# Kernel tuning notes

Measured on AMD Instinct MI355X. Metric: run time of the kernel, lower is better.

Reference implementation:

```python
import jax, jax.numpy as jnp
import numpy as np

N = 100000
E_RAND = 800000
IN_D, HID_D, OUT_D = 128, 64, 64
PROP_STEP = 8
ATTN_AFT = PROP_STEP // 2  # attention applied after this many prop steps
LAM = 1.0
ALP = 1.0 / (LAM + 1.0)    # alp=0 in init -> DGL auto-sets 1/(lam+1)
TAU = 0.2
P_RHO = 1.0
T_UP = -1.0                # T<=0 -> no upper threshold


def setup_inputs() -> dict:
    key = jax.random.key(0)
    k1, k2, k3, k4, k5 = jax.random.split(key, 5)
    loops = jnp.arange(N)
    src = jnp.concatenate([jax.random.randint(k1, (E_RAND,), 0, N), loops]).astype(jnp.int32)
    dst = jnp.concatenate([jax.random.randint(k2, (E_RAND,), 0, N), loops]).astype(jnp.int32)
    feat = jax.random.normal(k3, (N, IN_D), jnp.float32)
    # xavier_normal init, zero bias (as in MLP.reset_params)
    W_bef = jax.random.normal(k4, (IN_D, HID_D), jnp.float32) * np.float32(np.sqrt(2.0 / (IN_D + HID_D)))
    b_bef = jnp.zeros((HID_D,), jnp.float32)
    W_aft = jax.random.normal(k5, (HID_D, OUT_D), jnp.float32) * np.float32(np.sqrt(2.0 / (HID_D + OUT_D)))
    b_aft = jnp.zeros((OUT_D,), jnp.float32)
    return {"feat": feat, "W_bef": W_bef, "b_bef": b_bef, "W_aft": W_aft, "b_aft": b_aft, "src": src, "dst": dst}


def _ax(src, dst, w, X):
    # Y = A X with per-edge weights: scatter-add of w_e * X[src_e] into dst_e
    return jax.ops.segment_sum(X[src] * w[:, None], dst, num_segments=N)


def _attention(src, dst, Y):
    hs, hd = Y[src], Y[dst]  # [E, d]
    w = jnp.sum(hs * hs, -1) + jnp.sum(hd * hd, -1) - 2.0 * jnp.sum(hs * hd, -1)  # ||h_u - h_v||^2
    w = jax.nn.relu(w) + 1e-7
    w = jnp.power(w, 1.0 - 0.5 * P_RHO)
    w = jnp.maximum(w, TAU)  # lower threshold tau (in-place clamp in torch)
    if T_UP > 0:
        w = jnp.where(w > T_UP, jnp.inf, w)
    w = 1.0 / w + 1e-9
    deg = jax.ops.segment_sum(w, dst, num_segments=N)  # copy_e -> sum per dst node
    return w, deg


def _prop(src, dst, w, deg, Y, X):
    dt = LAM * deg + (1.0 - LAM)
    nrm = jnp.power(dt, -0.5)[:, None]
    py = nrm * _ax(src, dst, w, nrm * Y)
    return (1.0 - ALP) * Y + ALP * LAM * py + ALP * (X / dt[:, None])


def reference(feat, W_bef, b_bef, W_aft, b_aft, src, dst):
    X = feat @ W_bef + b_bef  # mlp_bef: single Linear(input_d, hidden_d)
    w = jnp.ones(src.shape[0], feat.dtype)  # initial edge weights = 1
    deg = jax.ops.segment_sum(w, dst, num_segments=N)  # in-degrees
    Y = X
    for k in range(PROP_STEP):
        Y = _prop(src, dst, w, deg, Y, X)
        if k == ATTN_AFT - 1:
            w, deg = _attention(src, dst, Y)
    # mlp_aft: init_activate=True (relu; norm='none', dropout=0) then Linear(hidden_d, output_d)
    return jax.nn.relu(Y) @ W_aft + b_aft
```

## Files before the change

kernel.cpp:

```cpp
#include <hip/hip_runtime.h>
#include <math.h>

#define IN_D 128
#define HID 64

typedef unsigned short ushort_t;
typedef unsigned int uint_t;

static __device__ __forceinline__ ushort_t f2bf(float f) {
    uint_t x = __float_as_uint(f);
    uint_t r = x + 0x7fffu + ((x >> 16) & 1u);
    return (ushort_t)(r >> 16);
}
static __device__ __forceinline__ float bf2f(ushort_t u) {
    return __uint_as_float(((uint_t)u) << 16);
}


__global__ void zero1_kernel(int* a, int n) {
    int i = blockIdx.x * blockDim.x + threadIdx.x;
    if (i < n) a[i] = 0;
}

__global__ void hist_kernel(const int* __restrict__ dst, int E, int* __restrict__ cnt) {
    int e = blockIdx.x * blockDim.x + threadIdx.x;
    if (e < E) atomicAdd(&cnt[dst[e]], 1);
}

__global__ void scan1_kernel(int* __restrict__ cnt, int N,
                             int* __restrict__ row_ptr, int* __restrict__ blocksum,
                             float* __restrict__ nrm, float* __restrict__ invdt) {
    __shared__ int sm[1024];
    int i = blockIdx.x * 1024 + threadIdx.x;
    int v = (i < N) ? cnt[i] : 0;
    if (i < N) {
        cnt[i] = 0;
        float d = (float)v;
        nrm[i] = 1.0f / sqrtf(d);
        invdt[i] = 1.0f / d;
    }
    sm[threadIdx.x] = v;
    __syncthreads();
    for (int off = 1; off < 1024; off <<= 1) {
        int t = (threadIdx.x >= off) ? sm[threadIdx.x - off] : 0;
        __syncthreads();
        sm[threadIdx.x] += t;
        __syncthreads();
    }
    if (i < N) row_ptr[i + 1] = sm[threadIdx.x];
    if (threadIdx.x == 1023) blocksum[blockIdx.x] = sm[1023];
}

__global__ void scan2_kernel(int* __restrict__ blocksum, int nb) {
    __shared__ int sm[1024];
    int v = (threadIdx.x < nb) ? blocksum[threadIdx.x] : 0;
    sm[threadIdx.x] = v;
    __syncthreads();
    for (int off = 1; off < 1024; off <<= 1) {
        int t = (threadIdx.x >= off) ? sm[threadIdx.x - off] : 0;
        __syncthreads();
        sm[threadIdx.x] += t;
        __syncthreads();
    }
    if (threadIdx.x < nb) blocksum[threadIdx.x] = sm[threadIdx.x] - v;
}

__global__ void scan3_kernel(int* __restrict__ row_ptr, int N, const int* __restrict__ blocksum) {
    int i = blockIdx.x * 1024 + threadIdx.x;
    if (i < N) row_ptr[i + 1] += blocksum[blockIdx.x];
    if (i == 0) row_ptr[0] = 0;
}

__global__ void scatter_kernel(const int* __restrict__ src, const int* __restrict__ dst, int E,
                               const int* __restrict__ row_ptr, int* __restrict__ cursor,
                               const float* __restrict__ nrm,
                               int* __restrict__ src_perm, int* __restrict__ dst_perm,
                               float* __restrict__ coef) {
    int e = blockIdx.x * blockDim.x + threadIdx.x;
    if (e < E) {
        int d = dst[e];
        int s = src[e];
        int pos = row_ptr[d] + atomicAdd(&cursor[d], 1);
        src_perm[pos] = s;
        dst_perm[pos] = d;
        coef[pos] = nrm[s];
    }
}

__global__ void coef_kernel(const int* __restrict__ src_perm, const float* __restrict__ w_perm,
                            const float* __restrict__ nrm, int E, float* __restrict__ coef) {
    int e = blockIdx.x * blockDim.x + threadIdx.x;
    if (e < E) coef[e] = w_perm[e] * nrm[src_perm[e]];
}


__global__ __launch_bounds__(256) void prop_kernel(
    const float* __restrict__ Yin, const ushort_t* __restrict__ Ybf,
    const float* __restrict__ X,
    const int* __restrict__ row_ptr, const int* __restrict__ src_perm,
    const float* __restrict__ coef, const float* __restrict__ nrm,
    const float* __restrict__ invdt, int N,
    float* __restrict__ Yout, ushort_t* __restrict__ Yout_bf) {
    int wave = __builtin_amdgcn_readfirstlane((blockIdx.x * blockDim.x + threadIdx.x) >> 6);
    int lane = threadIdx.x & 63;
    if (wave >= N) return;
    int r0 = row_ptr[wave], r1 = row_ptr[wave + 1];
    float acc = 0.0f;
    int j = r0;
    for (; j + 4 <= r1; j += 4) {
        float v[4], c[4];
        #pragma unroll
        for (int u = 0; u < 4; ++u) {
            int s = src_perm[j + u];
            c[u] = coef[j + u];
            v[u] = bf2f(Ybf[(size_t)s * HID + lane]);
        }
        #pragma unroll
        for (int u = 0; u < 4; ++u) acc = fmaf(c[u], v[u], acc);
    }
    if (j < r1) {
        float v[4], c[4];
        #pragma unroll
        for (int u = 0; u < 4; ++u) {
            int jj = j + u;
            int valid = jj < r1;
            int idx = valid ? jj : r1 - 1;
            int s = src_perm[idx];
            float cc = coef[idx];
            c[u] = valid ? cc : 0.0f;
            v[u] = bf2f(Ybf[(size_t)s * HID + lane]);
        }
        #pragma unroll
        for (int u = 0; u < 4; ++u) acc = fmaf(c[u], v[u], acc);
    }
    size_t base = (size_t)wave * HID + lane;
    float out = 0.5f * Yin[base] + (0.5f * nrm[wave]) * acc + (0.5f * invdt[wave]) * X[base];
    Yout[base] = out;
    Yout_bf[base] = f2bf(out);
}

__global__ __launch_bounds__(256) void attn_edge_kernel(
    const ushort_t* __restrict__ Ybf,
    const int* __restrict__ src_perm, const int* __restrict__ dst_perm,
    int E, float* __restrict__ w_perm) {
    int e = blockIdx.x * blockDim.x + threadIdx.x;
    if (e >= E) return;
    int s = src_perm[e], d = dst_perm[e];
    const uint4* ps = (const uint4*)(Ybf + (size_t)s * HID);
    const uint4* pd = (const uint4*)(Ybf + (size_t)d * HID);
    uint4 a[8], b[8];
    #pragma unroll
    for (int i = 0; i < 8; ++i) a[i] = ps[i];
    #pragma unroll
    for (int i = 0; i < 8; ++i) b[i] = pd[i];
    float ss = 0.0f;
    #pragma unroll
    for (int i = 0; i < 8; ++i) {
        const uint_t* ua = (const uint_t*)&a[i];
        const uint_t* ub = (const uint_t*)&b[i];
        #pragma unroll
        for (int j = 0; j < 4; ++j) {
            float slo = __uint_as_float(ua[j] << 16);
            float dlo = __uint_as_float(ub[j] << 16);
            float shi = __uint_as_float(ua[j] & 0xffff0000u);
            float dhi = __uint_as_float(ub[j] & 0xffff0000u);
            float t0 = slo - dlo;
            float t1 = shi - dhi;
            ss = fmaf(t0, t0, ss);
            ss = fmaf(t1, t1, ss);
        }
    }
    float w = fmaxf(ss, 0.0f) + 1e-7f;
    w = sqrtf(w);
    w = fmaxf(w, 0.2f);
    w = 1.0f / w + 1e-9f;
    w_perm[e] = w;
}

__global__ __launch_bounds__(256) void deg_sum_kernel(
    const float* __restrict__ w_perm, const int* __restrict__ row_ptr, int N,
    float* __restrict__ nrm, float* __restrict__ invdt) {
    int v = (blockIdx.x * blockDim.x + threadIdx.x) >> 6;
    int lane = threadIdx.x & 63;
    if (v >= N) return;
    int r0 = row_ptr[v], r1 = row_ptr[v + 1];
    float s = 0.0f;
    for (int j = r0 + lane; j < r1; j += 64) s += w_perm[j];
    #pragma unroll
    for (int o = 32; o >= 1; o >>= 1) s += __shfl_xor(s, o, 64);
    if (lane == 0) {
        nrm[v] = 1.0f / sqrtf(s);
        invdt[v] = 1.0f / s;
    }
}

__global__ __launch_bounds__(256) void gemm1_kernel(
    const float* __restrict__ feat, const float* __restrict__ W,
    const float* __restrict__ b, int N, float* __restrict__ X, ushort_t* __restrict__ Xbf) {
    __shared__ float Wl[IN_D * HID];
    __shared__ float featL[16 * IN_D];
    for (int i = threadIdx.x; i < IN_D * HID; i += 256) Wl[i] = W[i];
    int c = threadIdx.x & 63;
    int rsub = threadIdx.x >> 6;
    float bias = b[c];
    int ngroups = N / 16;
    const float4* feat4 = (const float4*)feat;
    for (int g = blockIdx.x; g < ngroups; g += gridDim.x) {
        __syncthreads();
        float4* fl4 = (float4*)featL;
        fl4[threadIdx.x]       = feat4[(size_t)g * 512 + threadIdx.x];
        fl4[threadIdx.x + 256] = feat4[(size_t)g * 512 + 256 + threadIdx.x];
        __syncthreads();
        const float4* f0 = (const float4*)&featL[(rsub) * IN_D];
        const float4* f1 = (const float4*)&featL[(rsub + 4) * IN_D];
        const float4* f2 = (const float4*)&featL[(rsub + 8) * IN_D];
        const float4* f3 = (const float4*)&featL[(rsub + 12) * IN_D];
        float acc0 = bias, acc1 = bias, acc2 = bias, acc3 = bias;
        #pragma unroll
        for (int k4 = 0; k4 < IN_D / 4; ++k4) {
            float4 a = f0[k4];
            float4 e = f1[k4];
            float4 h = f2[k4];
            float4 q = f3[k4];
            float w0 = Wl[(4 * k4 + 0) * HID + c];
            float w1 = Wl[(4 * k4 + 1) * HID + c];
            float w2 = Wl[(4 * k4 + 2) * HID + c];
            float w3 = Wl[(4 * k4 + 3) * HID + c];
            acc0 += a.x * w0 + a.y * w1 + a.z * w2 + a.w * w3;
            acc1 += e.x * w0 + e.y * w1 + e.z * w2 + e.w * w3;
            acc2 += h.x * w0 + h.y * w1 + h.z * w2 + h.w * w3;
            acc3 += q.x * w0 + q.y * w1 + q.z * w2 + q.w * w3;
        }
        size_t row = (size_t)g * 16;
        X[(row + rsub) * HID + c] = acc0;
        X[(row + rsub + 4) * HID + c] = acc1;
        X[(row + rsub + 8) * HID + c] = acc2;
        X[(row + rsub + 12) * HID + c] = acc3;
        Xbf[(row + rsub) * HID + c] = f2bf(acc0);
        Xbf[(row + rsub + 4) * HID + c] = f2bf(acc1);
        Xbf[(row + rsub + 8) * HID + c] = f2bf(acc2);
        Xbf[(row + rsub + 12) * HID + c] = f2bf(acc3);
    }
}

__global__ __launch_bounds__(256) void gemm2_kernel(
    const float* __restrict__ Y, const float* __restrict__ W,
    const float* __restrict__ b, int N, float* __restrict__ out) {
    __shared__ float Wl[HID * HID];
    __shared__ float Yl[16 * HID];
    for (int i = threadIdx.x; i < HID * HID; i += 256) Wl[i] = W[i];
    int c = threadIdx.x & 63;
    int rsub = threadIdx.x >> 6;
    float bias = b[c];
    int ngroups = N / 16;
    const float4* Y4 = (const float4*)Y;
    for (int g = blockIdx.x; g < ngroups; g += gridDim.x) {
        __syncthreads();
        {
            float4 v = Y4[(size_t)g * 256 + threadIdx.x];
            v.x = fmaxf(v.x, 0.0f); v.y = fmaxf(v.y, 0.0f);
            v.z = fmaxf(v.z, 0.0f); v.w = fmaxf(v.w, 0.0f);
            ((float4*)Yl)[threadIdx.x] = v;
        }
        __syncthreads();
        const float4* f0 = (const float4*)&Yl[(rsub) * HID];
        const float4* f1 = (const float4*)&Yl[(rsub + 4) * HID];
        const float4* f2 = (const float4*)&Yl[(rsub + 8) * HID];
        const float4* f3 = (const float4*)&Yl[(rsub + 12) * HID];
        float acc0 = bias, acc1 = bias, acc2 = bias, acc3 = bias;
        #pragma unroll
        for (int k4 = 0; k4 < HID / 4; ++k4) {
            float4 a = f0[k4];
            float4 e = f1[k4];
            float4 h = f2[k4];
            float4 q = f3[k4];
            float w0 = Wl[(4 * k4 + 0) * HID + c];
            float w1 = Wl[(4 * k4 + 1) * HID + c];
            float w2 = Wl[(4 * k4 + 2) * HID + c];
            float w3 = Wl[(4 * k4 + 3) * HID + c];
            acc0 += a.x * w0 + a.y * w1 + a.z * w2 + a.w * w3;
            acc1 += e.x * w0 + e.y * w1 + e.z * w2 + e.w * w3;
            acc2 += h.x * w0 + h.y * w1 + h.z * w2 + h.w * w3;
            acc3 += q.x * w0 + q.y * w1 + q.z * w2 + q.w * w3;
        }
        size_t row = (size_t)g * 16;
        out[(row + rsub) * HID + c] = acc0;
        out[(row + rsub + 4) * HID + c] = acc1;
        out[(row + rsub + 8) * HID + c] = acc2;
        out[(row + rsub + 12) * HID + c] = acc3;
    }
}


extern "C" void kernel_launch(void* const* d_in, const int* in_sizes, int n_in,
                              void* d_out, int out_size, void* d_ws, size_t ws_size,
                              hipStream_t stream) {
    const float* feat  = (const float*)d_in[0];
    const float* W_bef = (const float*)d_in[1];
    const float* b_bef = (const float*)d_in[2];
    const float* W_aft = (const float*)d_in[3];
    const float* b_aft = (const float*)d_in[4];
    const int*   src   = (const int*)d_in[5];
    const int*   dst   = (const int*)d_in[6];

    const int N = in_sizes[0] / IN_D;
    const int E = in_sizes[5];

    char* p = (char*)d_ws;
    auto alloc = [&](size_t bytes) -> void* {
        void* r = (void*)p;
        p += (bytes + 255) & ~(size_t)255;
        return r;
    };
    float*    X       = (float*)alloc((size_t)N * HID * 4);
    float*    Ya      = (float*)alloc((size_t)N * HID * 4);
    float*    Yb      = (float*)alloc((size_t)N * HID * 4);
    ushort_t* Xbf     = (ushort_t*)alloc((size_t)N * HID * 2);
    ushort_t* Yabf    = (ushort_t*)alloc((size_t)N * HID * 2);
    ushort_t* Ybbf    = (ushort_t*)alloc((size_t)N * HID * 2);
    int*      cnt     = (int*)alloc((size_t)N * 4);
    int*      row_ptr = (int*)alloc((size_t)(N + 1) * 4);
    int*      blocksum= (int*)alloc(4096);
    int*      src_perm= (int*)alloc((size_t)E * 4);
    int*      dst_perm= (int*)alloc((size_t)E * 4);
    float*    w_perm  = (float*)alloc((size_t)E * 4);
    float*    coef    = (float*)alloc((size_t)E * 4);
    float*    nrm     = (float*)alloc((size_t)N * 4);
    float*    invdt   = (float*)alloc((size_t)N * 4);

    const int TB = 256;
    dim3 blk(TB);
    int gN   = (N + TB - 1) / TB;
    int gE   = (E + TB - 1) / TB;
    int gNW  = (N * 64 + TB - 1) / TB;
    int nb   = (N + 1023) / 1024;

    zero1_kernel<<<gN, blk, 0, stream>>>(cnt, N);
    hist_kernel<<<gE, blk, 0, stream>>>(dst, E, cnt);
    scan1_kernel<<<nb, 1024, 0, stream>>>(cnt, N, row_ptr, blocksum, nrm, invdt);
    scan2_kernel<<<1, 1024, 0, stream>>>(blocksum, nb);
    scan3_kernel<<<nb, 1024, 0, stream>>>(row_ptr, N, blocksum);
    scatter_kernel<<<gE, blk, 0, stream>>>(src, dst, E, row_ptr, cnt, nrm,
                                           src_perm, dst_perm, coef);

    gemm1_kernel<<<2048, blk, 0, stream>>>(feat, W_bef, b_bef, N, X, Xbf);

    prop_kernel<<<gNW, blk, 0, stream>>>(X,  Xbf,  X, row_ptr, src_perm, coef, nrm, invdt, N, Ya, Yabf);
    prop_kernel<<<gNW, blk, 0, stream>>>(Ya, Yabf, X, row_ptr, src_perm, coef, nrm, invdt, N, Yb, Ybbf);
    prop_kernel<<<gNW, blk, 0, stream>>>(Yb, Ybbf, X, row_ptr, src_perm, coef, nrm, invdt, N, Ya, Yabf);
    prop_kernel<<<gNW, blk, 0, stream>>>(Ya, Yabf, X, row_ptr, src_perm, coef, nrm, invdt, N, Yb, Ybbf);

    attn_edge_kernel<<<gE, blk, 0, stream>>>(Ybbf, src_perm, dst_perm, E, w_perm);
    deg_sum_kernel<<<gNW, blk, 0, stream>>>(w_perm, row_ptr, N, nrm, invdt);
    coef_kernel<<<gE, blk, 0, stream>>>(src_perm, w_perm, nrm, E, coef);

    prop_kernel<<<gNW, blk, 0, stream>>>(Yb, Ybbf, X, row_ptr, src_perm, coef, nrm, invdt, N, Ya, Yabf);
    prop_kernel<<<gNW, blk, 0, stream>>>(Ya, Yabf, X, row_ptr, src_perm, coef, nrm, invdt, N, Yb, Ybbf);
    prop_kernel<<<gNW, blk, 0, stream>>>(Yb, Ybbf, X, row_ptr, src_perm, coef, nrm, invdt, N, Ya, Yabf);
    prop_kernel<<<gNW, blk, 0, stream>>>(Ya, Yabf, X, row_ptr, src_perm, coef, nrm, invdt, N, Yb, Ybbf);

    gemm2_kernel<<<512, blk, 0, stream>>>(Yb, W_aft, b_aft, N, (float*)d_out);
}
```

Measured before the change: 615.3 us.

## Prescale gathered features by source norm and precompute X term

```diff
diff --git a/kernel.cpp b/kernel.cpp
--- a/kernel.cpp
+++ b/kernel.cpp
@@ -73,81 +73,74 @@
 
 __global__ void scatter_kernel(const int* __restrict__ src, const int* __restrict__ dst, int E,
                                const int* __restrict__ row_ptr, int* __restrict__ cursor,
-                               const float* __restrict__ nrm,
-                               int* __restrict__ src_perm, int* __restrict__ dst_perm,
-                               float* __restrict__ coef) {
+                               int2* __restrict__ edges) {
     int e = blockIdx.x * blockDim.x + threadIdx.x;
     if (e < E) {
         int d = dst[e];
         int s = src[e];
         int pos = row_ptr[d] + atomicAdd(&cursor[d], 1);
-        src_perm[pos] = s;
-        dst_perm[pos] = d;
-        coef[pos] = nrm[s];
-    }
-}
-
-__global__ void coef_kernel(const int* __restrict__ src_perm, const float* __restrict__ w_perm,
-                            const float* __restrict__ nrm, int E, float* __restrict__ coef) {
-    int e = blockIdx.x * blockDim.x + threadIdx.x;
-    if (e < E) coef[e] = w_perm[e] * nrm[src_perm[e]];
-}
-
-
+        edges[pos] = make_int2(s, d);
+    }
+}
+
+
+template<bool USE_W>
 __global__ __launch_bounds__(256) void prop_kernel(
-    const float* __restrict__ Yin, const ushort_t* __restrict__ Ybf,
-    const float* __restrict__ X,
-    const int* __restrict__ row_ptr, const int* __restrict__ src_perm,
-    const float* __restrict__ coef, const float* __restrict__ nrm,
-    const float* __restrict__ invdt, int N,
-    float* __restrict__ Yout, ushort_t* __restrict__ Yout_bf) {
+    const float* __restrict__ Yin, const ushort_t* __restrict__ S,
+    const float* __restrict__ Z,
+    const int* __restrict__ row_ptr, const int2* __restrict__ edges,
+    const float* __restrict__ w_perm,
+    const float* __restrict__ nrm, int N,
+    float* __restrict__ Yout, ushort_t* __restrict__ Sout,
+    ushort_t* __restrict__ Uout) {
     int wave = __builtin_amdgcn_readfirstlane((blockIdx.x * blockDim.x + threadIdx.x) >> 6);
     int lane = threadIdx.x & 63;
     if (wave >= N) return;
     int r0 = row_ptr[wave], r1 = row_ptr[wave + 1];
     float acc = 0.0f;
     int j = r0;
-    for (; j + 4 <= r1; j += 4) {
-        float v[4], c[4];
-        #pragma unroll
-        for (int u = 0; u < 4; ++u) {
-            int s = src_perm[j + u];
-            c[u] = coef[j + u];
-            v[u] = bf2f(Ybf[(size_t)s * HID + lane]);
-        }
-        #pragma unroll
-        for (int u = 0; u < 4; ++u) acc = fmaf(c[u], v[u], acc);
+    for (; j + 8 <= r1; j += 8) {
+        float v[8], c[8];
+        #pragma unroll
+        for (int u = 0; u < 8; ++u) {
+            int s = edges[j + u].x;
+            v[u] = bf2f(S[(size_t)s * HID + lane]);
+            if (USE_W) c[u] = w_perm[j + u];
+        }
+        #pragma unroll
+        for (int u = 0; u < 8; ++u) acc = USE_W ? fmaf(c[u], v[u], acc) : (acc + v[u]);
     }
     if (j < r1) {
-        float v[4], c[4];
-        #pragma unroll
-        for (int u = 0; u < 4; ++u) {
+        float v[8], c[8];
+        #pragma unroll
+        for (int u = 0; u < 8; ++u) {
             int jj = j + u;
             int valid = jj < r1;
-            int idx = valid ? jj : r1 - 1;
-            int s = src_perm[idx];
-            float cc = coef[idx];
+            int idx = valid ? jj : r0;
+            int s = edges[idx].x;
+            v[u] = bf2f(S[(size_t)s * HID + lane]);
+            float cc = USE_W ? w_perm[idx] : 1.0f;
             c[u] = valid ? cc : 0.0f;
-            v[u] = bf2f(Ybf[(size_t)s * HID + lane]);
-        }
-        #pragma unroll
-        for (int u = 0; u < 4; ++u) acc = fmaf(c[u], v[u], acc);
+        }
+        #pragma unroll
+        for (int u = 0; u < 8; ++u) acc = fmaf(c[u], v[u], acc);
     }
     size_t base = (size_t)wave * HID + lane;
-    float out = 0.5f * Yin[base] + (0.5f * nrm[wave]) * acc + (0.5f * invdt[wave]) * X[base];
+    float nv = nrm[wave];
+    float out = 0.5f * Yin[base] + (0.5f * nv) * acc + Z[base];
     Yout[base] = out;
-    Yout_bf[base] = f2bf(out);
+    Sout[base] = f2bf(nv * out);
+    if (Uout) Uout[base] = f2bf(out);
 }
 
 __global__ __launch_bounds__(256) void attn_edge_kernel(
-    const ushort_t* __restrict__ Ybf,
-    const int* __restrict__ src_perm, const int* __restrict__ dst_perm,
+    const ushort_t* __restrict__ U, const int2* __restrict__ edges,
     int E, float* __restrict__ w_perm) {
     int e = blockIdx.x * blockDim.x + threadIdx.x;
     if (e >= E) return;
-    int s = src_perm[e], d = dst_perm[e];
-    const uint4* ps = (const uint4*)(Ybf + (size_t)s * HID);
-    const uint4* pd = (const uint4*)(Ybf + (size_t)d * HID);
+    int2 rec = edges[e];
+    const uint4* ps = (const uint4*)(U + (size_t)rec.x * HID);
+    const uint4* pd = (const uint4*)(U + (size_t)rec.y * HID);
     uint4 a[8], b[8];
     #pragma unroll
     for (int i = 0; i < 8; ++i) a[i] = ps[i];
@@ -177,10 +170,12 @@
     w_perm[e] = w;
 }
 
-__global__ __launch_bounds__(256) void deg_sum_kernel(
-    const float* __restrict__ w_perm, const int* __restrict__ row_ptr, int N,
-    float* __restrict__ nrm, float* __restrict__ invdt) {
-    int v = (blockIdx.x * blockDim.x + threadIdx.x) >> 6;
+__global__ __launch_bounds__(256) void deg_rescale_kernel(
+    const float* __restrict__ w_perm, const int* __restrict__ row_ptr,
+    const float* __restrict__ Y, const float* __restrict__ X, int N,
+    float* __restrict__ nrm, float* __restrict__ invdt,
+    ushort_t* __restrict__ S, float* __restrict__ Z) {
+    int v = __builtin_amdgcn_readfirstlane((blockIdx.x * blockDim.x + threadIdx.x) >> 6);
     int lane = threadIdx.x & 63;
     if (v >= N) return;
     int r0 = row_ptr[v], r1 = row_ptr[v + 1];
@@ -188,15 +183,19 @@
     for (int j = r0 + lane; j < r1; j += 64) s += w_perm[j];
     #pragma unroll
     for (int o = 32; o >= 1; o >>= 1) s += __shfl_xor(s, o, 64);
-    if (lane == 0) {
-        nrm[v] = 1.0f / sqrtf(s);
-        invdt[v] = 1.0f / s;
-    }
+    float nv = 1.0f / sqrtf(s);
+    float iv = 1.0f / s;
+    if (lane == 0) { nrm[v] = nv; invdt[v] = iv; }
+    size_t base = (size_t)v * HID + lane;
+    S[base] = f2bf(nv * Y[base]);
+    Z[base] = (0.5f * iv) * X[base];
 }
 
 __global__ __launch_bounds__(256) void gemm1_kernel(
     const float* __restrict__ feat, const float* __restrict__ W,
-    const float* __restrict__ b, int N, float* __restrict__ X, ushort_t* __restrict__ Xbf) {
+    const float* __restrict__ b, const float* __restrict__ nrm,
+    const float* __restrict__ invdt, int N,
+    float* __restrict__ X, ushort_t* __restrict__ S, float* __restrict__ Z) {
     __shared__ float Wl[IN_D * HID];
     __shared__ float featL[16 * IN_D];
     for (int i = threadIdx.x; i < IN_D * HID; i += 256) Wl[i] = W[i];
@@ -232,14 +231,19 @@
             acc3 += q.x * w0 + q.y * w1 + q.z * w2 + q.w * w3;
         }
         size_t row = (size_t)g * 16;
-        X[(row + rsub) * HID + c] = acc0;
-        X[(row + rsub + 4) * HID + c] = acc1;
-        X[(row + rsub + 8) * HID + c] = acc2;
-        X[(row + rsub + 12) * HID + c] = acc3;
-        Xbf[(row + rsub) * HID + c] = f2bf(acc0);
-        Xbf[(row + rsub + 4) * HID + c] = f2bf(acc1);
-        Xbf[(row + rsub + 8) * HID + c] = f2bf(acc2);
-        Xbf[(row + rsub + 12) * HID + c] = f2bf(acc3);
+        int r0i = row + rsub, r1i = row + rsub + 4, r2i = row + rsub + 8, r3i = row + rsub + 12;
+        X[(size_t)r0i * HID + c] = acc0;
+        X[(size_t)r1i * HID + c] = acc1;
+        X[(size_t)r2i * HID + c] = acc2;
+        X[(size_t)r3i * HID + c] = acc3;
+        S[(size_t)r0i * HID + c] = f2bf(nrm[r0i] * acc0);
+        S[(size_t)r1i * HID + c] = f2bf(nrm[r1i] * acc1);
+        S[(size_t)r2i * HID + c] = f2bf(nrm[r2i] * acc2);
+        S[(size_t)r3i * HID + c] = f2bf(nrm[r3i] * acc3);
+        Z[(size_t)r0i * HID + c] = 0.5f * invdt[r0i] * acc0;
+        Z[(size_t)r1i * HID + c] = 0.5f * invdt[r1i] * acc1;
+        Z[(size_t)r2i * HID + c] = 0.5f * invdt[r2i] * acc2;
+        Z[(size_t)r3i * HID + c] = 0.5f * invdt[r3i] * acc3;
     }
 }
 
@@ -315,16 +319,16 @@
     float*    X       = (float*)alloc((size_t)N * HID * 4);
     float*    Ya      = (float*)alloc((size_t)N * HID * 4);
     float*    Yb      = (float*)alloc((size_t)N * HID * 4);
-    ushort_t* Xbf     = (ushort_t*)alloc((size_t)N * HID * 2);
-    ushort_t* Yabf    = (ushort_t*)alloc((size_t)N * HID * 2);
-    ushort_t* Ybbf    = (ushort_t*)alloc((size_t)N * HID * 2);
+    float*    Z       = (float*)alloc((size_t)N * HID * 4);
+    ushort_t* Sx      = (ushort_t*)alloc((size_t)N * HID * 2);
+    ushort_t* Sa      = (ushort_t*)alloc((size_t)N * HID * 2);
+    ushort_t* Sb      = (ushort_t*)alloc((size_t)N * HID * 2);
+    ushort_t* U       = (ushort_t*)alloc((size_t)N * HID * 2);
     int*      cnt     = (int*)alloc((size_t)N * 4);
     int*      row_ptr = (int*)alloc((size_t)(N + 1) * 4);
     int*      blocksum= (int*)alloc(4096);
-    int*      src_perm= (int*)alloc((size_t)E * 4);
-    int*      dst_perm= (int*)alloc((size_t)E * 4);
+    int2*     edges   = (int2*)alloc((size_t)E * 8);
     float*    w_perm  = (float*)alloc((size_t)E * 4);
-    float*    coef    = (float*)alloc((size_t)E * 4);
     float*    nrm     = (float*)alloc((size_t)N * 4);
     float*    invdt   = (float*)alloc((size_t)N * 4);
 
@@ -340,24 +344,22 @@
     scan1_kernel<<<nb, 1024, 0, stream>>>(cnt, N, row_ptr, blocksum, nrm, invdt);
     scan2_kernel<<<1, 1024, 0, stream>>>(blocksum, nb);
     scan3_kernel<<<nb, 1024, 0, stream>>>(row_ptr, N, blocksum);
-    scatter_kernel<<<gE, blk, 0, stream>>>(src, dst, E, row_ptr, cnt, nrm,
-                                           src_perm, dst_perm, coef);
-
-    gemm1_kernel<<<2048, blk, 0, stream>>>(feat, W_bef, b_bef, N, X, Xbf);
-
-    prop_kernel<<<gNW, blk, 0, stream>>>(X,  Xbf,  X, row_ptr, src_perm, coef, nrm, invdt, N, Ya, Yabf);
-    prop_kernel<<<gNW, blk, 0, stream>>>(Ya, Yabf, X, row_ptr, src_perm, coef, nrm, invdt, N, Yb, Ybbf);
-    prop_kernel<<<gNW, blk, 0, stream>>>(Yb, Ybbf, X, row_ptr, src_perm, coef, nrm, invdt, N, Ya, Yabf);
-    prop_kernel<<<gNW, blk, 0, stream>>>(Ya, Yabf, X, row_ptr, src_perm, coef, nrm, invdt, N, Yb, Ybbf);
-
-    attn_edge_kernel<<<gE, blk, 0, stream>>>(Ybbf, src_perm, dst_perm, E, w_perm);
-    deg_sum_kernel<<<gNW, blk, 0, stream>>>(w_perm, row_ptr, N, nrm, invdt);
-    coef_kernel<<<gE, blk, 0, stream>>>(src_perm, w_perm, nrm, E, coef);
-
-    prop_kernel<<<gNW, blk, 0, stream>>>(Yb, Ybbf, X, row_ptr, src_perm, coef, nrm, invdt, N, Ya, Yabf);
-    prop_kernel<<<gNW, blk, 0, stream>>>(Ya, Yabf, X, row_ptr, src_perm, coef, nrm, invdt, N, Yb, Ybbf);
-    prop_kernel<<<gNW, blk, 0, stream>>>(Yb, Ybbf, X, row_ptr, src_perm, coef, nrm, invdt, N, Ya, Yabf);
-    prop_kernel<<<gNW, blk, 0, stream>>>(Ya, Yabf, X, row_ptr, src_perm, coef, nrm, invdt, N, Yb, Ybbf);
+    scatter_kernel<<<gE, blk, 0, stream>>>(src, dst, E, row_ptr, cnt, edges);
+
+    gemm1_kernel<<<2048, blk, 0, stream>>>(feat, W_bef, b_bef, nrm, invdt, N, X, Sx, Z);
+
+    prop_kernel<false><<<gNW, blk, 0, stream>>>(X,  Sx, Z, row_ptr, edges, nullptr, nrm, N, Ya, Sa, nullptr);
+    prop_kernel<false><<<gNW, blk, 0, stream>>>(Ya, Sa, Z, row_ptr, edges, nullptr, nrm, N, Yb, Sb, nullptr);
+    prop_kernel<false><<<gNW, blk, 0, stream>>>(Yb, Sb, Z, row_ptr, edges, nullptr, nrm, N, Ya, Sa, nullptr);
+    prop_kernel<false><<<gNW, blk, 0, stream>>>(Ya, Sa, Z, row_ptr, edges, nullptr, nrm, N, Yb, Sb, U);
+
+    attn_edge_kernel<<<gE, blk, 0, stream>>>(U, edges, E, w_perm);
+    deg_rescale_kernel<<<gNW, blk, 0, stream>>>(w_perm, row_ptr, Yb, X, N, nrm, invdt, Sb, Z);
+
+    prop_kernel<true><<<gNW, blk, 0, stream>>>(Yb, Sb, Z, row_ptr, edges, w_perm, nrm, N, Ya, Sa, nullptr);
+    prop_kernel<true><<<gNW, blk, 0, stream>>>(Ya, Sa, Z, row_ptr, edges, w_perm, nrm, N, Yb, Sb, nullptr);
+    prop_kernel<true><<<gNW, blk, 0, stream>>>(Yb, Sb, Z, row_ptr, edges, w_perm, nrm, N, Ya, Sa, nullptr);
+    prop_kernel<true><<<gNW, blk, 0, stream>>>(Ya, Sa, Z, row_ptr, edges, w_perm, nrm, N, Yb, Sb, nullptr);
 
     gemm2_kernel<<<512, blk, 0, stream>>>(Yb, W_aft, b_aft, N, (float*)d_out);
 }
```

Result: no change. 618.7 us (+0.5%).
